# Optimization experiments

Hardware: AMD Instinct MI355X
Metric: run time of the kernel (lower is better)

Reference implementation:

```python
import jax, jax.numpy as jnp
import numpy as np

NEG_SLOPE = 0.2


def gat_conv(x, edge_index, W, att_src, att_dst, bias, heads, out_ch):
    """PyG GATConv (add_self_loops=True, concat=True) in jax.
    x: [N, F_in], edge_index: [2, E] (row0=src j, row1=dst i).
    Returns [N, heads*out_ch].
    """
    N = x.shape[0]
    # add self loops (PyG default)
    loops = jnp.tile(jnp.arange(N, dtype=edge_index.dtype)[None, :], (2, 1))
    ei = jnp.concatenate([edge_index, loops], axis=1)
    src, dst = ei[0], ei[1]
    h = (x @ W).reshape(N, heads, out_ch)              # [N,H,C]
    a_src = (h * att_src).sum(-1)                      # [N,H]
    a_dst = (h * att_dst).sum(-1)                      # [N,H]
    alpha = jax.nn.leaky_relu(a_src[src] + a_dst[dst], NEG_SLOPE)  # [E,H]
    # segment softmax over destination nodes
    amax = jax.ops.segment_max(alpha, dst, num_segments=N)         # [N,H]
    ealpha = jnp.exp(alpha - amax[dst])
    denom = jax.ops.segment_sum(ealpha, dst, num_segments=N)
    alpha = ealpha / jnp.maximum(denom, 1e-16)[dst]
    msg = h[src] * alpha[..., None]                    # [E,H,C]
    out = jax.ops.segment_sum(msg, dst, num_segments=N)  # [N,H,C]
    return out.reshape(N, heads * out_ch) + bias


def setup_inputs() -> dict:
    key = jax.random.key(0)
    ks = jax.random.split(key, 16)
    N, F_in, E, E_lab, Fe = 10000, 128, 160000, 100000, 16
    H1, C = 4, 128  # gat1 heads, hidden_dim
    inp = {
        "x": jax.random.normal(ks[0], (N, F_in), jnp.float32),
        "edge_index": jax.random.randint(ks[1], (2, E), 0, N, jnp.int64),
        "edge_attr": jax.random.normal(ks[2], (E, Fe), jnp.float32),
        "edge_label_index": jax.random.randint(ks[3], (2, E_lab), 0, N, jnp.int64),
        "edge_label_attr": jax.random.normal(ks[4], (E_lab, Fe), jnp.float32),
        # gat1 params
        "W1": jax.random.normal(ks[5], (F_in, H1 * C), jnp.float32) / np.sqrt(F_in),
        "att_src1": jax.random.normal(ks[6], (1, H1, C), jnp.float32) / np.sqrt(C),
        "att_dst1": jax.random.normal(ks[7], (1, H1, C), jnp.float32) / np.sqrt(C),
        "b1": jnp.zeros((H1 * C,), jnp.float32),
        # gat2 params (heads=1)
        "W2": jax.random.normal(ks[8], (H1 * C, C), jnp.float32) / np.sqrt(H1 * C),
        "att_src2": jax.random.normal(ks[9], (1, 1, C), jnp.float32) / np.sqrt(C),
        "att_dst2": jax.random.normal(ks[10], (1, 1, C), jnp.float32) / np.sqrt(C),
        "b2": jnp.zeros((C,), jnp.float32),
        # edge MLP: actual input dim = C + Fe = 144 (see notes)
        "mlp_w1": jax.random.normal(ks[11], (C + Fe, 64), jnp.float32) / np.sqrt(C + Fe),
        "mlp_b1": jnp.zeros((64,), jnp.float32),
        "mlp_w2": jax.random.normal(ks[12], (64, 2), jnp.float32) / np.sqrt(64.0),
        "mlp_b2": jnp.zeros((2,), jnp.float32),
    }
    return inp


def reference(x, edge_index, edge_attr, edge_label_index, edge_label_attr,
              W1, att_src1, att_dst1, b1, W2, att_src2, att_dst2, b2,
              mlp_w1, mlp_b1, mlp_w2, mlp_b2):
    # edge_attr is unused by the original forward (GATConv called without it)
    h = jax.nn.elu(gat_conv(x, edge_index, W1, att_src1, att_dst1, b1, heads=4, out_ch=128))
    h = jax.nn.elu(gat_conv(h, edge_index, W2, att_src2, att_dst2, b2, heads=1, out_ch=128))
    edge_src = h[edge_label_index[0]]
    edge_dst = h[edge_label_index[1]]
    edge_emb = edge_src * edge_dst                     # [E_lab, 128]
    feats = jnp.concatenate([edge_emb, edge_label_attr], axis=1)
    out = jax.nn.relu(feats @ mlp_w1 + mlp_b1) @ mlp_w2 + mlp_b2
    return out
```

## Files before the change

kernel.cpp:

```cpp
#include <hip/hip_runtime.h>
#include <hip/hip_bf16.h>
#include <cstdint>

typedef __attribute__((ext_vector_type(8))) short bf16x8;
typedef __attribute__((ext_vector_type(4))) float f32x4;

__device__ __forceinline__ float lrelu02(float x){ return x > 0.f ? x : 0.2f*x; }
__device__ __forceinline__ float elu1(float x){ return x > 0.f ? x : __expf(x)-1.f; }
__device__ __forceinline__ unsigned short bf16_rne(float f){
  unsigned int u = __float_as_uint(f);
  u += 0x7FFFu + ((u >> 16) & 1u);
  return (unsigned short)(u >> 16);
}
__device__ __forceinline__ float b2f(unsigned int hi16){ return __uint_as_float(hi16 << 16); }
__device__ __forceinline__ unsigned int packbf(float a, float b){
  return (unsigned int)bf16_rne(a) | ((unsigned int)bf16_rne(b) << 16);
}

__device__ __forceinline__ float wave_reduce_sum(float v){
  #pragma unroll
  for (int o = 32; o >= 1; o >>= 1) v += __shfl_xor(v, o, 64);
  return v;
}

__global__ void hist_kernel(const int* __restrict__ ei, int* __restrict__ cnt, int E){
  int e = blockIdx.x*blockDim.x + threadIdx.x;
  if (e < E) atomicAdd(&cnt[ei[E + e]], 1);
}

__global__ void scan_kernel(const int* __restrict__ cnt, int* __restrict__ rp, int N){
  __shared__ int part[1024];
  const int PER = 16;
  int t = threadIdx.x;
  int base = t*PER;
  int local[PER]; int s = 0;
  #pragma unroll
  for (int i=0;i<PER;i++){ int idx=base+i; int v = (idx<N)? cnt[idx] : 0; local[i]=s; s+=v; }
  part[t]=s; __syncthreads();
  for (int off=1; off<1024; off<<=1){
    int v = (t>=off)? part[t-off] : 0;
    __syncthreads();
    part[t] += v;
    __syncthreads();
  }
  int ex = (t>0)? part[t-1] : 0;
  #pragma unroll
  for (int i=0;i<PER;i++){ int idx=base+i; if (idx<N) rp[idx] = ex + local[i]; }
  if (t==0) rp[N] = part[1023];
}

__global__ void fill_kernel(const int* __restrict__ ei, const int* __restrict__ rp,
                            int* __restrict__ fl, int* __restrict__ col, int E){
  int e = blockIdx.x*blockDim.x + threadIdx.x;
  if (e >= E) return;
  int d = ei[E+e];
  int pos = rp[d] + atomicAdd(&fl[d], 1);
  col[pos] = ei[e];
}

__global__ void conv_all_kernel(const float* __restrict__ x, unsigned short* __restrict__ xb,
                                const float* __restrict__ W1, unsigned short* __restrict__ W1t,
                                const float* __restrict__ W2, unsigned short* __restrict__ W2t,
                                const float* __restrict__ mw1, unsigned short* __restrict__ mw1t){
  int t = blockIdx.x*256 + threadIdx.x;
  if (t < 320000){
    int i = t*4;
    float4 v = *(const float4*)(x + i);
    xb[i+0] = bf16_rne(v.x); xb[i+1] = bf16_rne(v.y);
    xb[i+2] = bf16_rne(v.z); xb[i+3] = bf16_rne(v.w);
  } else if (t < 385536){
    int i = t - 320000;
    int n = i >> 7, k = i & 127;
    W1t[i] = bf16_rne(W1[(size_t)k*512 + n]);
  } else if (t < 451072){
    int i = t - 385536;
    int n = i >> 9, k = i & 511;
    W2t[i] = bf16_rne(W2[(size_t)k*128 + n]);
  } else if (t < 461312){
    int i = t - 451072;
    int n = i / 160, k = i % 160;
    mw1t[i] = (k < 144) ? bf16_rne(mw1[(size_t)k*64 + n]) : (unsigned short)0;
  }
}

template<int BN, int SPLITK, int RELU, int WB, int OUTB>
__global__ __launch_bounds__(256) void mgemm_kernel(
    const unsigned short* __restrict__ A,
    const unsigned short* __restrict__ Bt,
    const float* __restrict__ bias,
    void* __restrict__ C,
    int M, int N, int K){
  const int BM = 128, BK = 32, LDP = BK + 8;
  const int NF = BN/32;
  __shared__ unsigned short As[BM*LDP];
  __shared__ unsigned short Bs[BN*LDP];
  int tid = threadIdx.x;
  int lane = tid & 63, wid = tid >> 6;
  int wr = wid >> 1, wc = wid & 1;
  int row0 = blockIdx.y*BM, col0 = blockIdx.x*BN;
  int kchunk = K / SPLITK;
  int k0base = blockIdx.z * kchunk;
  f32x4 acc[4][NF];
  #pragma unroll
  for (int m=0;m<4;m++)
    #pragma unroll
    for (int n=0;n<NF;n++) acc[m][n] = (f32x4){0.f,0.f,0.f,0.f};

  for (int kt = 0; kt < kchunk; kt += BK){
    int k0 = k0base + kt;
    #pragma unroll
    for (int i=0;i<(BM*4)/256;i++){
      int li = i*256 + tid;
      int r = li >> 2, q = li & 3;
      int gr = row0 + r;
      uint4 v = make_uint4(0u,0u,0u,0u);
      if (gr < M) v = *(const uint4*)(A + (size_t)gr*K + k0 + q*8);
      *(uint4*)(&As[r*LDP + q*8]) = v;
    }
    #pragma unroll
    for (int i=0;i<(BN*4)/256;i++){
      int li = i*256 + tid;
      int r = li >> 2, q = li & 3;
      int gn = col0 + r;
      uint4 v = make_uint4(0u,0u,0u,0u);
      if (gn < N) v = *(const uint4*)(Bt + (size_t)gn*K + k0 + q*8);
      *(uint4*)(&Bs[r*LDP + q*8]) = v;
    }
    __syncthreads();
    int kq = (lane >> 4) * 8;
    bf16x8 af[4], bfr[NF];
    #pragma unroll
    for (int m=0;m<4;m++)
      af[m] = *(const bf16x8*)(&As[(wr*64 + m*16 + (lane&15))*LDP + kq]);
    #pragma unroll
    for (int n=0;n<NF;n++)
      bfr[n] = *(const bf16x8*)(&Bs[(wc*(BN/2) + n*16 + (lane&15))*LDP + kq]);
    #pragma unroll
    for (int m=0;m<4;m++)
      #pragma unroll
      for (int n=0;n<NF;n++)
        acc[m][n] = __builtin_amdgcn_mfma_f32_16x16x32_bf16(af[m], bfr[n], acc[m][n], 0, 0, 0);
    __syncthreads();
  }
  #pragma unroll
  for (int m=0;m<4;m++){
    #pragma unroll
    for (int j=0;j<4;j++){
      int r = row0 + wr*64 + m*16 + (lane>>4)*4 + j;
      if (r >= M) continue;
      #pragma unroll
      for (int n=0;n<NF;n++){
        int c = col0 + wc*(BN/2) + n*16 + (lane&15);
        float v = acc[m][n][j];
        if (WB) v += bias[c];
        if (RELU) v = fmaxf(v, 0.f);
        if (OUTB){
          ((unsigned short*)C)[(size_t)r*N + c] = bf16_rne(v);
        } else {
          float* Cb = (float*)C + (size_t)blockIdx.z * M * N;
          Cb[(size_t)r*N + c] = v;
        }
      }
    }
  }
}

__global__ __launch_bounds__(256) void mgemm_mlp2_kernel(
    const unsigned short* __restrict__ A,
    const unsigned short* __restrict__ Bt,
    const float* __restrict__ mb1,
    const float* __restrict__ w2,
    const float* __restrict__ b2,
    float* __restrict__ out, int M){
  const int BK = 32, LDP = BK + 8, K = 160;
  __shared__ unsigned short As[128*LDP];
  __shared__ unsigned short Bs[64*LDP];
  __shared__ float hid[128][65];
  __shared__ float w2s[128];
  int tid = threadIdx.x;
  int lane = tid & 63, wid = tid >> 6;
  int wr = wid >> 1, wc = wid & 1;
  int row0 = blockIdx.y*128;
  if (tid < 128) w2s[tid] = w2[tid];
  f32x4 acc[4][2];
  #pragma unroll
  for (int m=0;m<4;m++){ acc[m][0] = (f32x4){0,0,0,0}; acc[m][1] = (f32x4){0,0,0,0}; }

  for (int k0 = 0; k0 < K; k0 += BK){
    #pragma unroll
    for (int i=0;i<2;i++){
      int li = i*256 + tid;
      int r = li >> 2, q = li & 3;
      int gr = row0 + r;
      uint4 v = make_uint4(0u,0u,0u,0u);
      if (gr < M) v = *(const uint4*)(A + (size_t)gr*K + k0 + q*8);
      *(uint4*)(&As[r*LDP + q*8]) = v;
    }
    {
      int r = tid >> 2, q = tid & 3;
      uint4 v = *(const uint4*)(Bt + (size_t)r*K + k0 + q*8);
      *(uint4*)(&Bs[r*LDP + q*8]) = v;
    }
    __syncthreads();
    int kq = (lane >> 4) * 8;
    bf16x8 af[4], bfr[2];
    #pragma unroll
    for (int m=0;m<4;m++)
      af[m] = *(const bf16x8*)(&As[(wr*64 + m*16 + (lane&15))*LDP + kq]);
    #pragma unroll
    for (int n=0;n<2;n++)
      bfr[n] = *(const bf16x8*)(&Bs[(wc*32 + n*16 + (lane&15))*LDP + kq]);
    #pragma unroll
    for (int m=0;m<4;m++)
      #pragma unroll
      for (int n=0;n<2;n++)
        acc[m][n] = __builtin_amdgcn_mfma_f32_16x16x32_bf16(af[m], bfr[n], acc[m][n], 0, 0, 0);
    __syncthreads();
  }
  #pragma unroll
  for (int m=0;m<4;m++){
    #pragma unroll
    for (int j=0;j<4;j++){
      int r = wr*64 + m*16 + (lane>>4)*4 + j;
      #pragma unroll
      for (int n=0;n<2;n++){
        int c = wc*32 + n*16 + (lane&15);
        hid[r][c] = fmaxf(acc[m][n][j] + mb1[c], 0.f);
      }
    }
  }
  __syncthreads();
  int r = tid >> 1, hf = tid & 1;
  int cbase = hf*32;
  float p0 = 0.f, p1 = 0.f;
  #pragma unroll
  for (int c=0;c<32;c++){
    float v = hid[r][cbase + c];
    p0 += v * w2s[(cbase + c)*2 + 0];
    p1 += v * w2s[(cbase + c)*2 + 1];
  }
  p0 += __shfl_xor(p0, 1, 64);
  p1 += __shfl_xor(p1, 1, 64);
  if (hf == 0 && row0 + r < M){
    out[(size_t)(row0 + r)*2 + 0] = p0 + b2[0];
    out[(size_t)(row0 + r)*2 + 1] = p1 + b2[1];
  }
}

__global__ void reduce4b_attn_kernel(const float4* __restrict__ p, uint2* __restrict__ o,
                                     const float* __restrict__ as2, const float* __restrict__ ad2,
                                     float* __restrict__ asrc, float* __restrict__ adst,
                                     int N, int s4){
  int idx = blockIdx.x*256 + threadIdx.x;
  int n = idx >> 5;
  if (n >= N) return;
  float4 a = p[idx], b = p[idx+s4], c = p[idx+2*s4], d = p[idx+3*s4];
  float rx = a.x+b.x+c.x+d.x, ry = a.y+b.y+c.y+d.y;
  float rz = a.z+b.z+c.z+d.z, rw = a.w+b.w+c.w+d.w;
  o[idx] = make_uint2(packbf(rx, ry), packbf(rz, rw));
  int c4 = (idx & 31)*4;
  float ps = rx*as2[c4] + ry*as2[c4+1] + rz*as2[c4+2] + rw*as2[c4+3];
  float pd = rx*ad2[c4] + ry*ad2[c4+1] + rz*ad2[c4+2] + rw*ad2[c4+3];
  #pragma unroll
  for (int off=1; off<32; off<<=1){ ps += __shfl_xor(ps,off,64); pd += __shfl_xor(pd,off,64); }
  if ((idx & 31) == 0){ asrc[n] = ps; adst[n] = pd; }
}

__global__ void attn4_kernel(const unsigned short* __restrict__ h,
                             const float* __restrict__ att_src,
                             const float* __restrict__ att_dst,
                             float* __restrict__ asrc, float* __restrict__ adst, int N){
  int lane = threadIdx.x & 63;
  int n = blockIdx.x*4 + (threadIdx.x >> 6);
  if (n >= N) return;
  const uint4* hp = (const uint4*)(h + (size_t)n*512);
  uint4 u = hp[lane];
  int ch = lane*8;
  float f0 = b2f(u.x & 0xffffu), f1 = b2f(u.x >> 16);
  float f2 = b2f(u.y & 0xffffu), f3 = b2f(u.y >> 16);
  float f4 = b2f(u.z & 0xffffu), f5 = b2f(u.z >> 16);
  float f6 = b2f(u.w & 0xffffu), f7 = b2f(u.w >> 16);
  float s = f0*att_src[ch+0] + f1*att_src[ch+1] + f2*att_src[ch+2] + f3*att_src[ch+3]
          + f4*att_src[ch+4] + f5*att_src[ch+5] + f6*att_src[ch+6] + f7*att_src[ch+7];
  float d = f0*att_dst[ch+0] + f1*att_dst[ch+1] + f2*att_dst[ch+2] + f3*att_dst[ch+3]
          + f4*att_dst[ch+4] + f5*att_dst[ch+5] + f6*att_dst[ch+6] + f7*att_dst[ch+7];
  #pragma unroll
  for (int o=1; o<16; o<<=1){ s += __shfl_xor(s, o, 64); d += __shfl_xor(d, o, 64); }
  if ((lane & 15) == 0){
    int hh = lane >> 4;
    asrc[n*4 + hh] = s; adst[n*4 + hh] = d;
  }
}

__global__ void agg4_kernel(const unsigned short* __restrict__ h,
                            const float* __restrict__ asrc,
                            const float* __restrict__ adst,
                            const float* __restrict__ bias,
                            const int* __restrict__ rp,
                            const int* __restrict__ col,
                            unsigned short* __restrict__ outb, int N){
  int lane = threadIdx.x & 63;
  int n = blockIdx.x*4 + (threadIdx.x >> 6);
  if (n >= N) return;
  int hh = lane >> 4;
  int beg = rp[n], end = rp[n+1];
  float adst_i = adst[n*4 + hh];
  float wself = __expf(lrelu02(asrc[n*4 + hh] + adst_i));
  const uint4* hp = (const uint4*)(h + (size_t)n*512);
  uint4 us = hp[lane];
  float a0 = b2f(us.x & 0xffffu)*wself, a1 = b2f(us.x >> 16)*wself;
  float a2 = b2f(us.y & 0xffffu)*wself, a3 = b2f(us.y >> 16)*wself;
  float a4 = b2f(us.z & 0xffffu)*wself, a5 = b2f(us.z >> 16)*wself;
  float a6 = b2f(us.w & 0xffffu)*wself, a7 = b2f(us.w >> 16)*wself;
  float wsum = wself;

  int e = beg;
  for (; e + 8 <= end; e += 8){
    int s0 = col[e],   s1 = col[e+1], s2 = col[e+2], s3 = col[e+3];
    int s4 = col[e+4], s5 = col[e+5], s6 = col[e+6], s7 = col[e+7];
    uint4 u0 = ((const uint4*)(h + (size_t)s0*512))[lane];
    uint4 u1 = ((const uint4*)(h + (size_t)s1*512))[lane];
    uint4 u2 = ((const uint4*)(h + (size_t)s2*512))[lane];
    uint4 u3 = ((const uint4*)(h + (size_t)s3*512))[lane];
    uint4 u4 = ((const uint4*)(h + (size_t)s4*512))[lane];
    uint4 u5 = ((const uint4*)(h + (size_t)s5*512))[lane];
    uint4 u6 = ((const uint4*)(h + (size_t)s6*512))[lane];
    uint4 u7 = ((const uint4*)(h + (size_t)s7*512))[lane];
    float w0 = __expf(lrelu02(asrc[s0*4 + hh] + adst_i));
    float w1 = __expf(lrelu02(asrc[s1*4 + hh] + adst_i));
    float w2 = __expf(lrelu02(asrc[s2*4 + hh] + adst_i));
    float w3 = __expf(lrelu02(asrc[s3*4 + hh] + adst_i));
    float w4 = __expf(lrelu02(asrc[s4*4 + hh] + adst_i));
    float w5 = __expf(lrelu02(asrc[s5*4 + hh] + adst_i));
    float w6 = __expf(lrelu02(asrc[s6*4 + hh] + adst_i));
    float w7 = __expf(lrelu02(asrc[s7*4 + hh] + adst_i));
    wsum += w0 + w1 + w2 + w3 + w4 + w5 + w6 + w7;
    a0 += b2f(u0.x & 0xffffu)*w0; a1 += b2f(u0.x >> 16)*w0;
    a2 += b2f(u0.y & 0xffffu)*w0; a3 += b2f(u0.y >> 16)*w0;
    a4 += b2f(u0.z & 0xffffu)*w0; a5 += b2f(u0.z >> 16)*w0;
    a6 += b2f(u0.w & 0xffffu)*w0; a7 += b2f(u0.w >> 16)*w0;
    a0 += b2f(u1.x & 0xffffu)*w1; a1 += b2f(u1.x >> 16)*w1;
    a2 += b2f(u1.y & 0xffffu)*w1; a3 += b2f(u1.y >> 16)*w1;
    a4 += b2f(u1.z & 0xffffu)*w1; a5 += b2f(u1.z >> 16)*w1;
    a6 += b2f(u1.w & 0xffffu)*w1; a7 += b2f(u1.w >> 16)*w1;
    a0 += b2f(u2.x & 0xffffu)*w2; a1 += b2f(u2.x >> 16)*w2;
    a2 += b2f(u2.y & 0xffffu)*w2; a3 += b2f(u2.y >> 16)*w2;
    a4 += b2f(u2.z & 0xffffu)*w2; a5 += b2f(u2.z >> 16)*w2;
    a6 += b2f(u2.w & 0xffffu)*w2; a7 += b2f(u2.w >> 16)*w2;
    a0 += b2f(u3.x & 0xffffu)*w3; a1 += b2f(u3.x >> 16)*w3;
    a2 += b2f(u3.y & 0xffffu)*w3; a3 += b2f(u3.y >> 16)*w3;
    a4 += b2f(u3.z & 0xffffu)*w3; a5 += b2f(u3.z >> 16)*w3;
    a6 += b2f(u3.w & 0xffffu)*w3; a7 += b2f(u3.w >> 16)*w3;
    a0 += b2f(u4.x & 0xffffu)*w4; a1 += b2f(u4.x >> 16)*w4;
    a2 += b2f(u4.y & 0xffffu)*w4; a3 += b2f(u4.y >> 16)*w4;
    a4 += b2f(u4.z & 0xffffu)*w4; a5 += b2f(u4.z >> 16)*w4;
    a6 += b2f(u4.w & 0xffffu)*w4; a7 += b2f(u4.w >> 16)*w4;
    a0 += b2f(u5.x & 0xffffu)*w5; a1 += b2f(u5.x >> 16)*w5;
    a2 += b2f(u5.y & 0xffffu)*w5; a3 += b2f(u5.y >> 16)*w5;
    a4 += b2f(u5.z & 0xffffu)*w5; a5 += b2f(u5.z >> 16)*w5;
    a6 += b2f(u5.w & 0xffffu)*w5; a7 += b2f(u5.w >> 16)*w5;
    a0 += b2f(u6.x & 0xffffu)*w6; a1 += b2f(u6.x >> 16)*w6;
    a2 += b2f(u6.y & 0xffffu)*w6; a3 += b2f(u6.y >> 16)*w6;
    a4 += b2f(u6.z & 0xffffu)*w6; a5 += b2f(u6.z >> 16)*w6;
    a6 += b2f(u6.w & 0xffffu)*w6; a7 += b2f(u6.w >> 16)*w6;
    a0 += b2f(u7.x & 0xffffu)*w7; a1 += b2f(u7.x >> 16)*w7;
    a2 += b2f(u7.y & 0xffffu)*w7; a3 += b2f(u7.y >> 16)*w7;
    a4 += b2f(u7.z & 0xffffu)*w7; a5 += b2f(u7.z >> 16)*w7;
    a6 += b2f(u7.w & 0xffffu)*w7; a7 += b2f(u7.w >> 16)*w7;
  }
  for (; e + 4 <= end; e += 4){
    int s0 = col[e], s1 = col[e+1], s2 = col[e+2], s3 = col[e+3];
    uint4 u0 = ((const uint4*)(h + (size_t)s0*512))[lane];
    uint4 u1 = ((const uint4*)(h + (size_t)s1*512))[lane];
    uint4 u2 = ((const uint4*)(h + (size_t)s2*512))[lane];
    uint4 u3 = ((const uint4*)(h + (size_t)s3*512))[lane];
    float w0 = __expf(lrelu02(asrc[s0*4 + hh] + adst_i));
    float w1 = __expf(lrelu02(asrc[s1*4 + hh] + adst_i));
    float w2 = __expf(lrelu02(asrc[s2*4 + hh] + adst_i));
    float w3 = __expf(lrelu02(asrc[s3*4 + hh] + adst_i));
    wsum += w0 + w1 + w2 + w3;
    a0 += b2f(u0.x & 0xffffu)*w0; a1 += b2f(u0.x >> 16)*w0;
    a2 += b2f(u0.y & 0xffffu)*w0; a3 += b2f(u0.y >> 16)*w0;
    a4 += b2f(u0.z & 0xffffu)*w0; a5 += b2f(u0.z >> 16)*w0;
    a6 += b2f(u0.w & 0xffffu)*w0; a7 += b2f(u0.w >> 16)*w0;
    a0 += b2f(u1.x & 0xffffu)*w1; a1 += b2f(u1.x >> 16)*w1;
    a2 += b2f(u1.y & 0xffffu)*w1; a3 += b2f(u1.y >> 16)*w1;
    a4 += b2f(u1.z & 0xffffu)*w1; a5 += b2f(u1.z >> 16)*w1;
    a6 += b2f(u1.w & 0xffffu)*w1; a7 += b2f(u1.w >> 16)*w1;
    a0 += b2f(u2.x & 0xffffu)*w2; a1 += b2f(u2.x >> 16)*w2;
    a2 += b2f(u2.y & 0xffffu)*w2; a3 += b2f(u2.y >> 16)*w2;
    a4 += b2f(u2.z & 0xffffu)*w2; a5 += b2f(u2.z >> 16)*w2;
    a6 += b2f(u2.w & 0xffffu)*w2; a7 += b2f(u2.w >> 16)*w2;
    a0 += b2f(u3.x & 0xffffu)*w3; a1 += b2f(u3.x >> 16)*w3;
    a2 += b2f(u3.y & 0xffffu)*w3; a3 += b2f(u3.y >> 16)*w3;
    a4 += b2f(u3.z & 0xffffu)*w3; a5 += b2f(u3.z >> 16)*w3;
    a6 += b2f(u3.w & 0xffffu)*w3; a7 += b2f(u3.w >> 16)*w3;
  }
  for (; e < end; ++e){
    int s0 = col[e];
    uint4 u0 = ((const uint4*)(h + (size_t)s0*512))[lane];
    float w0 = __expf(lrelu02(asrc[s0*4 + hh] + adst_i));
    wsum += w0;
    a0 += b2f(u0.x & 0xffffu)*w0; a1 += b2f(u0.x >> 16)*w0;
    a2 += b2f(u0.y & 0xffffu)*w0; a3 += b2f(u0.y >> 16)*w0;
    a4 += b2f(u0.z & 0xffffu)*w0; a5 += b2f(u0.z >> 16)*w0;
    a6 += b2f(u0.w & 0xffffu)*w0; a7 += b2f(u0.w >> 16)*w0;
  }
  float inv = 1.f / fmaxf(wsum, 1e-16f);
  int ch = lane*8;
  float o0 = elu1(a0*inv + bias[ch+0]);
  float o1 = elu1(a1*inv + bias[ch+1]);
  float o2 = elu1(a2*inv + bias[ch+2]);
  float o3 = elu1(a3*inv + bias[ch+3]);
  float o4 = elu1(a4*inv + bias[ch+4]);
  float o5 = elu1(a5*inv + bias[ch+5]);
  float o6 = elu1(a6*inv + bias[ch+6]);
  float o7 = elu1(a7*inv + bias[ch+7]);
  ((uint4*)(outb + (size_t)n*512))[lane] =
      make_uint4(packbf(o0,o1), packbf(o2,o3), packbf(o4,o5), packbf(o6,o7));
}

__global__ void agg1_kernel(const unsigned short* __restrict__ h,
                            const float* __restrict__ asrc,
                            const float* __restrict__ adst,
                            const float* __restrict__ bias,
                            const int* __restrict__ rp,
                            const int* __restrict__ col,
                            unsigned short* __restrict__ outb, int N){
  const int C = 128;
  int lane = threadIdx.x & 63;
  int n = blockIdx.x*4 + (threadIdx.x >> 6);
  if (n >= N) return;
  int beg = rp[n], end = rp[n+1];
  float adst_i = adst[n];
  float wself = __expf(lrelu02(asrc[n] + adst_i));
  const unsigned int* hp = (const unsigned int*)(h + (size_t)n*C);
  unsigned int us = hp[lane];
  float acc0 = b2f(us & 0xffffu)*wself, acc1 = b2f(us >> 16)*wself;
  float wsum = wself;

  int e = beg;
  for (; e + 4 <= end; e += 4){
    int r0 = col[e], r1 = col[e+1], r2 = col[e+2], r3 = col[e+3];
    const unsigned int* q0 = (const unsigned int*)(h + (size_t)r0*C);
    const unsigned int* q1 = (const unsigned int*)(h + (size_t)r1*C);
    const unsigned int* q2 = (const unsigned int*)(h + (size_t)r2*C);
    const unsigned int* q3 = (const unsigned int*)(h + (size_t)r3*C);
    unsigned int u0 = q0[lane], u1 = q1[lane], u2 = q2[lane], u3 = q3[lane];
    float w0 = __expf(lrelu02(asrc[r0] + adst_i));
    float w1 = __expf(lrelu02(asrc[r1] + adst_i));
    float w2 = __expf(lrelu02(asrc[r2] + adst_i));
    float w3 = __expf(lrelu02(asrc[r3] + adst_i));
    wsum += w0 + w1 + w2 + w3;
    acc0 += b2f(u0 & 0xffffu)*w0; acc1 += b2f(u0 >> 16)*w0;
    acc0 += b2f(u1 & 0xffffu)*w1; acc1 += b2f(u1 >> 16)*w1;
    acc0 += b2f(u2 & 0xffffu)*w2; acc1 += b2f(u2 >> 16)*w2;
    acc0 += b2f(u3 & 0xffffu)*w3; acc1 += b2f(u3 >> 16)*w3;
  }
  for (; e < end; ++e){
    int r0 = col[e];
    const unsigned int* q0 = (const unsigned int*)(h + (size_t)r0*C);
    unsigned int u0 = q0[lane];
    float w0 = __expf(lrelu02(asrc[r0] + adst_i));
    wsum += w0;
    acc0 += b2f(u0 & 0xffffu)*w0; acc1 += b2f(u0 >> 16)*w0;
  }
  float inv = 1.f / fmaxf(wsum, 1e-16f);
  int c0 = 2*lane;
  float o0 = elu1(acc0*inv + bias[c0]);
  float o1 = elu1(acc1*inv + bias[c0+1]);
  ((unsigned int*)outb)[(size_t)n*(C/2) + lane] = packbf(o0, o1);
}

__global__ void feats_kernel(const unsigned short* __restrict__ hf, const int* __restrict__ eli,
                             const float* __restrict__ attr, unsigned short* __restrict__ feats, int E){
  int lane = threadIdx.x & 63;
  int e = blockIdx.x*4 + (threadIdx.x >> 6);
  if (e >= E) return;
  int s = eli[e], d = eli[E+e];
  const unsigned int* hs = (const unsigned int*)(hf + (size_t)s*128);
  const unsigned int* hd = (const unsigned int*)(hf + (size_t)d*128);
  unsigned int us = hs[lane], ud = hd[lane];
  float p0 = b2f(us & 0xffffu) * b2f(ud & 0xffffu);
  float p1 = b2f(us >> 16)     * b2f(ud >> 16);
  unsigned int* ft = (unsigned int*)(feats + (size_t)e*160);
  ft[lane] = packbf(p0, p1);
  if (lane < 8){
    float a0 = attr[(size_t)e*16 + 2*lane], a1 = attr[(size_t)e*16 + 2*lane + 1];
    ft[64+lane] = packbf(a0, a1);
  } else if (lane < 16){
    ft[64+lane] = 0u;
  }
}

extern "C" void kernel_launch(void* const* d_in, const int* in_sizes, int n_in,
                              void* d_out, int out_size, void* d_ws, size_t ws_size,
                              hipStream_t stream){
  const float* x    = (const float*)d_in[0];
  const int*   ei   = (const int*)d_in[1];
  const int*   eli  = (const int*)d_in[3];
  const float* attr = (const float*)d_in[4];
  const float* W1   = (const float*)d_in[5];
  const float* as1  = (const float*)d_in[6];
  const float* ad1  = (const float*)d_in[7];
  const float* b1   = (const float*)d_in[8];
  const float* W2   = (const float*)d_in[9];
  const float* as2  = (const float*)d_in[10];
  const float* ad2  = (const float*)d_in[11];
  const float* b2   = (const float*)d_in[12];
  const float* mw1  = (const float*)d_in[13];
  const float* mb1  = (const float*)d_in[14];
  const float* mw2  = (const float*)d_in[15];
  const float* mb2  = (const float*)d_in[16];
  float* out = (float*)d_out;

  const int N  = in_sizes[0]/128;
  const int E  = in_sizes[1]/2;
  const int EL = in_sizes[3]/2;
  const int H1 = 4, C = 128;
  const int K1 = 128, N1 = 512;
  const int K2 = 512, N2 = 128;
  const int K3 = 160, N3 = 64;

  char* ws = (char*)d_ws;
  auto al = [](size_t x){ return (x + 255) & ~(size_t)255; };
  size_t off = 0;
  unsigned short* W1t  = (unsigned short*)(ws + off); off += al((size_t)N1*K1*2);
  unsigned short* W2t  = (unsigned short*)(ws + off); off += al((size_t)N2*K2*2);
  unsigned short* mw1t = (unsigned short*)(ws + off); off += al((size_t)N3*K3*2);
  float* asrc1 = (float*)(ws + off); off += al((size_t)N*H1*4);
  float* adst1 = (float*)(ws + off); off += al((size_t)N*H1*4);
  float* asrc2 = (float*)(ws + off); off += al((size_t)N*4);
  float* adst2 = (float*)(ws + off); off += al((size_t)N*4);
  int* cnt = (int*)(ws + off); off += (size_t)N*4;
  int* fl  = (int*)(ws + off); off += al((size_t)N*4);
  int* rp  = (int*)(ws + off); off += al((size_t)(N+1)*4);
  int* col = (int*)(ws + off); off += al((size_t)E*4);
  unsigned short* out2b = (unsigned short*)(ws + off); off += al((size_t)N*C*2);
  size_t A0 = off;
  unsigned short* xb    = (unsigned short*)(ws + A0);
  unsigned short* h1    = (unsigned short*)(ws + A0 + al((size_t)N*K1*2));
  unsigned short* out1b = (unsigned short*)((char*)h1 + al((size_t)N*N1*2));
  float*          part  = (float*)((char*)out1b + al((size_t)N*N1*2));
  unsigned short* h2b   = (unsigned short*)((char*)part + al((size_t)4*N*N2*4));
  unsigned short* featsb = (unsigned short*)(ws + A0);

  hipMemsetAsync(cnt, 0, (size_t)2*N*4, stream);
  hist_kernel<<<(E+255)/256, 256, 0, stream>>>(ei, cnt, E);
  scan_kernel<<<1, 1024, 0, stream>>>(cnt, rp, N);
  fill_kernel<<<(E+255)/256, 256, 0, stream>>>(ei, rp, fl, col, E);

  conv_all_kernel<<<1803, 256, 0, stream>>>(x, xb, W1, W1t, W2, W2t, mw1, mw1t);

  mgemm_kernel<64,1,0,0,1><<<dim3(N1/64, (N+127)/128, 1), 256, 0, stream>>>(
      xb, W1t, nullptr, h1, N, N1, K1);
  attn4_kernel<<<(N+3)/4, 256, 0, stream>>>(h1, as1, ad1, asrc1, adst1, N);
  agg4_kernel<<<(N+3)/4, 256, 0, stream>>>(h1, asrc1, adst1, b1, rp, col, out1b, N);

  mgemm_kernel<64,4,0,0,0><<<dim3(N2/64, (N+127)/128, 4), 256, 0, stream>>>(
      out1b, W2t, nullptr, part, N, N2, K2);
  reduce4b_attn_kernel<<<(N*32+255)/256, 256, 0, stream>>>(
      (const float4*)part, (uint2*)h2b, as2, ad2, asrc2, adst2, N, N*N2/4);
  agg1_kernel<<<(N+3)/4, 256, 0, stream>>>(h2b, asrc2, adst2, b2, rp, col, out2b, N);

  feats_kernel<<<(EL+3)/4, 256, 0, stream>>>(out2b, eli, attr, featsb, EL);
  mgemm_mlp2_kernel<<<dim3(1, (EL+127)/128, 1), 256, 0, stream>>>(
      featsb, mw1t, mb1, mw2, mb2, out, EL);
}
```

Baseline: 146.9 us.

## Fuse edge-feature gather into the edge MLP GEMM A-tile load

Removes the separate feats kernel and builds each A tile of the edge MLP GEMM on the fly. The tile comes from the gathered source and destination node embeddings (their bf16 product) plus the converted edge attributes, with the remaining columns zero-padded. This avoids writing and re-reading a 100k x 160 bf16 intermediate and saves one kernel launch. In exchange the GEMM's load phase now does scattered gathers and conversion arithmetic in the K loop, which may increase latency per tile.

```diff
diff --git a/kernel.cpp b/kernel.cpp
--- a/kernel.cpp
+++ b/kernel.cpp
@@ -166,7 +166,9 @@
 }
 
 __global__ __launch_bounds__(256) void mgemm_mlp2_kernel(
-    const unsigned short* __restrict__ A,
+    const unsigned short* __restrict__ hf,
+    const int* __restrict__ eli,
+    const float* __restrict__ attr,
     const unsigned short* __restrict__ Bt,
     const float* __restrict__ mb1,
     const float* __restrict__ w2,
@@ -182,20 +184,43 @@
   int wr = wid >> 1, wc = wid & 1;
   int row0 = blockIdx.y*128;
   if (tid < 128) w2s[tid] = w2[tid];
+
+  int r0_ = tid >> 2, q_ = tid & 3;
+  int r1_ = 64 + r0_;
+  int gr0 = row0 + r0_, gr1 = row0 + r1_;
+  bool ok0 = gr0 < M, ok1 = gr1 < M;
+  int s0=0, d0=0, s1=0, d1=0;
+  if (ok0){ s0 = eli[gr0]; d0 = eli[M + gr0]; }
+  if (ok1){ s1 = eli[gr1]; d1 = eli[M + gr1]; }
+
+  auto make_chunk = [&](int s, int d, int gr, bool ok, int k) -> uint4 {
+    uint4 v = make_uint4(0u,0u,0u,0u);
+    if (!ok) return v;
+    if (k < 128){
+      uint4 a = *(const uint4*)(hf + (size_t)s*128 + k);
+      uint4 b = *(const uint4*)(hf + (size_t)d*128 + k);
+      v.x = packbf(b2f(a.x & 0xffffu)*b2f(b.x & 0xffffu), b2f(a.x >> 16)*b2f(b.x >> 16));
+      v.y = packbf(b2f(a.y & 0xffffu)*b2f(b.y & 0xffffu), b2f(a.y >> 16)*b2f(b.y >> 16));
+      v.z = packbf(b2f(a.z & 0xffffu)*b2f(b.z & 0xffffu), b2f(a.z >> 16)*b2f(b.z >> 16));
+      v.w = packbf(b2f(a.w & 0xffffu)*b2f(b.w & 0xffffu), b2f(a.w >> 16)*b2f(b.w >> 16));
+    } else if (k < 144){
+      const float* pa = attr + (size_t)gr*16 + (k - 128);
+      float4 x0 = *(const float4*)pa;
+      float4 x1 = *(const float4*)(pa + 4);
+      v.x = packbf(x0.x, x0.y); v.y = packbf(x0.z, x0.w);
+      v.z = packbf(x1.x, x1.y); v.w = packbf(x1.z, x1.w);
+    }
+    return v;
+  };
+
   f32x4 acc[4][2];
   #pragma unroll
   for (int m=0;m<4;m++){ acc[m][0] = (f32x4){0,0,0,0}; acc[m][1] = (f32x4){0,0,0,0}; }
 
   for (int k0 = 0; k0 < K; k0 += BK){
-    #pragma unroll
-    for (int i=0;i<2;i++){
-      int li = i*256 + tid;
-      int r = li >> 2, q = li & 3;
-      int gr = row0 + r;
-      uint4 v = make_uint4(0u,0u,0u,0u);
-      if (gr < M) v = *(const uint4*)(A + (size_t)gr*K + k0 + q*8);
-      *(uint4*)(&As[r*LDP + q*8]) = v;
-    }
+    int k = k0 + q_*8;
+    *(uint4*)(&As[r0_*LDP + q_*8]) = make_chunk(s0, d0, gr0, ok0, k);
+    *(uint4*)(&As[r1_*LDP + q_*8]) = make_chunk(s1, d1, gr1, ok1, k);
     {
       int r = tid >> 2, q = tid & 3;
       uint4 v = *(const uint4*)(Bt + (size_t)r*K + k0 + q*8);
@@ -230,8 +255,8 @@
     }
   }
   __syncthreads();
-  int r = tid >> 1, hf = tid & 1;
-  int cbase = hf*32;
+  int r = tid >> 1, hf2 = tid & 1;
+  int cbase = hf2*32;
   float p0 = 0.f, p1 = 0.f;
   #pragma unroll
   for (int c=0;c<32;c++){
@@ -241,7 +266,7 @@
   }
   p0 += __shfl_xor(p0, 1, 64);
   p1 += __shfl_xor(p1, 1, 64);
-  if (hf == 0 && row0 + r < M){
+  if (hf2 == 0 && row0 + r < M){
     out[(size_t)(row0 + r)*2 + 0] = p0 + b2[0];
     out[(size_t)(row0 + r)*2 + 1] = p1 + b2[1];
   }
@@ -472,27 +497,6 @@
   ((unsigned int*)outb)[(size_t)n*(C/2) + lane] = packbf(o0, o1);
 }
 
-__global__ void feats_kernel(const unsigned short* __restrict__ hf, const int* __restrict__ eli,
-                             const float* __restrict__ attr, unsigned short* __restrict__ feats, int E){
-  int lane = threadIdx.x & 63;
-  int e = blockIdx.x*4 + (threadIdx.x >> 6);
-  if (e >= E) return;
-  int s = eli[e], d = eli[E+e];
-  const unsigned int* hs = (const unsigned int*)(hf + (size_t)s*128);
-  const unsigned int* hd = (const unsigned int*)(hf + (size_t)d*128);
-  unsigned int us = hs[lane], ud = hd[lane];
-  float p0 = b2f(us & 0xffffu) * b2f(ud & 0xffffu);
-  float p1 = b2f(us >> 16)     * b2f(ud >> 16);
-  unsigned int* ft = (unsigned int*)(feats + (size_t)e*160);
-  ft[lane] = packbf(p0, p1);
-  if (lane < 8){
-    float a0 = attr[(size_t)e*16 + 2*lane], a1 = attr[(size_t)e*16 + 2*lane + 1];
-    ft[64+lane] = packbf(a0, a1);
-  } else if (lane < 16){
-    ft[64+lane] = 0u;
-  }
-}
-
 extern "C" void kernel_launch(void* const* d_in, const int* in_sizes, int n_in,
                               void* d_out, int out_size, void* d_ws, size_t ws_size,
                               hipStream_t stream){
@@ -543,7 +547,6 @@
   unsigned short* out1b = (unsigned short*)((char*)h1 + al((size_t)N*N1*2));
   float*          part  = (float*)((char*)out1b + al((size_t)N*N1*2));
   unsigned short* h2b   = (unsigned short*)((char*)part + al((size_t)4*N*N2*4));
-  unsigned short* featsb = (unsigned short*)(ws + A0);
 
   hipMemsetAsync(cnt, 0, (size_t)2*N*4, stream);
   hist_kernel<<<(E+255)/256, 256, 0, stream>>>(ei, cnt, E);
@@ -563,7 +566,6 @@
       (const float4*)part, (uint2*)h2b, as2, ad2, asrc2, adst2, N, N*N2/4);
   agg1_kernel<<<(N+3)/4, 256, 0, stream>>>(h2b, asrc2, adst2, b2, rp, col, out2b, N);
 
-  feats_kernel<<<(EL+3)/4, 256, 0, stream>>>(out2b, eli, attr, featsb, EL);
   mgemm_mlp2_kernel<<<dim3(1, (EL+127)/128, 1), 256, 0, stream>>>(
-      featsb, mw1t, mb1, mw2, mb2, out, EL);
-}
+      out2b, eli, attr, mw1t, mb1, mw2, mb2, out, EL);
+}
```

Measured after the change: 129.6 us. 11.8% less time.
